# Performance work log

Measured on AMD Instinct MI355X. Metric: run time of the kernel, lower is better.

## Reference

```python
import jax, jax.numpy as jnp
import numpy as np
from jax import lax

EPS = 1e-6


def _gaussian_blur(heatmaps, kernel_size):
    # heatmaps: (B, K, H, W). 2D Gaussian conv with 'same' padding, as in the torch code.
    if kernel_size % 2 == 0:
        kernel_size += 1
    B, K, H, W = heatmaps.shape
    sigma = (kernel_size - 1) / 6.0
    coords = jnp.arange(kernel_size, dtype=heatmaps.dtype) - (kernel_size - 1) / 2.0
    g = jnp.exp(-coords ** 2 / (2 * sigma ** 2))
    g = g / g.sum()
    kernel = (g[None, :] * g[:, None])[None, None]  # (1,1,ks,ks)
    pad = kernel_size // 2
    x = heatmaps.reshape(B * K, 1, H, W)
    out = lax.conv_general_dilated(
        x, kernel, window_strides=(1, 1), padding=[(pad, pad), (pad, pad)],
        dimension_numbers=('NCHW', 'OIHW', 'NCHW'))
    return out.reshape(B, K, H, W)


def _dark_forward(heatmaps, kernel_size):
    B, K, H, W = heatmaps.shape
    smooth = _gaussian_blur(heatmaps, kernel_size)
    flat = smooth.reshape(B, K, H * W)
    max_idx = jnp.argmax(flat, axis=-1)            # (B,K) int
    max_vals = jnp.max(flat, axis=-1)              # (B,K)
    y_int = max_idx // W
    x_int = max_idx % W

    # Gather 3x3 patches around the peak (clipped indices; invalid peaks masked below).
    off = jnp.arange(-1, 2)
    yy = jnp.clip(y_int[..., None, None] + off[:, None], 0, H - 1)   # (B,K,3,3)
    xx = jnp.clip(x_int[..., None, None] + off[None, :], 0, W - 1)   # (B,K,3,3)
    lin = (yy * W + xx).reshape(B, K, 9)
    p = jnp.take_along_axis(flat, lin, axis=-1).reshape(B, K, 3, 3)

    dx = (p[..., 1, 2] - p[..., 1, 0]) * 0.5
    dy = (p[..., 2, 1] - p[..., 0, 1]) * 0.5
    dxx = p[..., 1, 2] - 2.0 * p[..., 1, 1] + p[..., 1, 0]
    dyy = p[..., 2, 1] - 2.0 * p[..., 1, 1] + p[..., 0, 1]
    dxy = (p[..., 2, 2] - p[..., 2, 0] - p[..., 0, 2] + p[..., 0, 0]) * 0.25
    det = dxx * dyy - dxy * dxy

    boundary_ok = (x_int >= 1) & (x_int < W - 1) & (y_int >= 1) & (y_int < H - 1)
    valid = boundary_ok & (jnp.abs(det) >= EPS) & (dxx < 0)
    safe_det = jnp.where(valid, det, 1.0)
    off_x = jnp.where(valid, jnp.clip(-(dyy * dx - dxy * dy) / safe_det, -0.5, 0.5), 0.0)
    off_y = jnp.where(valid, jnp.clip(-(dxx * dy - dxy * dx) / safe_det, -0.5, 0.5), 0.0)

    x = jnp.clip(x_int.astype(heatmaps.dtype) + off_x, 0, W - 1)
    y = jnp.clip(y_int.astype(heatmaps.dtype) + off_y, 0, H - 1)
    coords = jnp.stack([x, y], axis=-1)            # (B,K,2)
    return coords, max_vals


def setup_inputs() -> dict:
    key = jax.random.key(0)
    heatmaps = jax.random.normal(key, (64, 17, 256, 192), dtype=jnp.float32)
    return {"heatmaps": heatmaps, "kernel_size": 11}


def reference(heatmaps, kernel_size):
    return _dark_forward(heatmaps, kernel_size)
```

## Files before the change

kernel.cpp:

```cpp
#include <hip/hip_runtime.h>
#include <math.h>

#define H 256
#define W 192
#define BK 1088
#define KS 11
#define QROWS 64

struct GaussW { float g[KS]; };

__global__ __launch_bounds__(192) void dark_scan(const float* __restrict__ hm,
                                                 float* __restrict__ wsv,
                                                 int* __restrict__ wsi,
                                                 GaussW gw) {
  const int bid = blockIdx.x;
  const int q   = bid & 3;
  const int mg  = bid >> 2;
  const int t   = threadIdx.x;
  const int ml  = t / 48;
  const int cg  = t % 48;
  const int map = mg * 4 + ml;
  const int col0 = cg * 4;
  const float* base = hm + (size_t)map * (H * W);

  __shared__ float vbuf[4][208];
  __shared__ float rv[192];
  __shared__ int   ri[192];

  for (int i = t; i < 4 * 208; i += 192) ((float*)vbuf)[i] = 0.f;
  __syncthreads();

  const int y0 = q * QROWS;
  const int rs = (q == 0) ? 0 : (y0 - 5);
  const int re = y0 + QROWS + 4;

  float4 w[KS];
  #pragma unroll
  for (int i = 0; i < KS; ++i) w[i] = make_float4(0.f, 0.f, 0.f, 0.f);

  float bestv = -INFINITY;
  int   besti = 0x7fffffff;

  for (int rb = rs; rb <= re; rb += KS) {
    #pragma unroll
    for (int s = 0; s < KS; ++s) {
      const int rr = rb + s;
      if (rr <= re) {
        float4 raw;
        if (rr < H) raw = *(const float4*)(base + rr * W + col0);
        else        raw = make_float4(0.f, 0.f, 0.f, 0.f);
        w[s] = raw;
        if (rr >= y0 + 5) {
          float4 v = make_float4(0.f, 0.f, 0.f, 0.f);
          #pragma unroll
          for (int i = 0; i < KS; ++i) {
            const float4 wi = w[(s + 1 + i) % KS];
            const float gi = gw.g[i];
            v.x = fmaf(gi, wi.x, v.x);
            v.y = fmaf(gi, wi.y, v.y);
            v.z = fmaf(gi, wi.z, v.z);
            v.w = fmaf(gi, wi.w, v.w);
          }
          *(float4*)(&vbuf[ml][8 + col0]) = v;
          __syncthreads();
          const float* vb = &vbuf[ml][0];
          float a[20];
          *(float4*)(a + 0)  = *(const float4*)(vb + col0);
          *(float4*)(a + 4)  = *(const float4*)(vb + col0 + 4);
          *(float4*)(a + 8)  = *(const float4*)(vb + col0 + 8);
          *(float4*)(a + 12) = *(const float4*)(vb + col0 + 12);
          *(float4*)(a + 16) = *(const float4*)(vb + col0 + 16);
          const int y = rr - 5;
          #pragma unroll
          for (int c = 0; c < 4; ++c) {
            float hv = 0.f;
            #pragma unroll
            for (int j = 0; j < KS; ++j) hv = fmaf(gw.g[j], a[3 + c + j], hv);
            const int idx = y * W + col0 + c;
            if (hv > bestv) { bestv = hv; besti = idx; }
          }
          __syncthreads();
        }
      }
    }
  }

  rv[t] = bestv; ri[t] = besti;
  __syncthreads();
  if (cg == 0) {
    float bv = -INFINITY; int bi = 0x7fffffff;
    for (int k = 0; k < 48; ++k) {
      const float v = rv[ml * 48 + k]; const int ix = ri[ml * 48 + k];
      if (v > bv || (v == bv && ix < bi)) { bv = v; bi = ix; }
    }
    wsv[map * 4 + q] = bv;
    wsi[map * 4 + q] = bi;
  }
}

__global__ __launch_bounds__(64) void dark_decode(const float* __restrict__ hm,
                                                  const float* __restrict__ wsv,
                                                  const int* __restrict__ wsi,
                                                  float* __restrict__ out,
                                                  GaussW gw) {
  const int j = blockIdx.x;
  const int t = threadIdx.x;
  __shared__ float sv[4]; __shared__ int si[4];
  __shared__ float hbuf[39];
  __shared__ int sxy[3];
  __shared__ float sbv;

  if (t < 4) { sv[t] = wsv[j * 4 + t]; si[t] = wsi[j * 4 + t]; }
  __syncthreads();
  if (t == 0) {
    float bv = sv[0]; int bi = si[0];
    for (int k = 1; k < 4; ++k)
      if (sv[k] > bv || (sv[k] == bv && si[k] < bi)) { bv = sv[k]; bi = si[k]; }
    const int y = bi / W; const int x = bi - y * W;
    sxy[0] = x; sxy[1] = y;
    sxy[2] = (x >= 1 && x < W - 1 && y >= 1 && y < H - 1) ? 1 : 0;
    sbv = bv;
  }
  __syncthreads();
  const int x = sxy[0], y = sxy[1], interior = sxy[2];

  if (interior && t < 39) {
    const int rl = t / 3, dxc = t % 3;
    const int rr = y - 6 + rl;
    const int cc = x - 1 + dxc;
    float hv = 0.f;
    if (rr >= 0 && rr < H) {
      const float* rowp = hm + (size_t)j * (H * W) + rr * W;
      #pragma unroll
      for (int k = 0; k < KS; ++k) {
        const int c2 = cc - 5 + k;
        const float vv = (c2 >= 0 && c2 < W) ? rowp[c2] : 0.f;
        hv = fmaf(gw.g[k], vv, hv);
      }
    }
    hbuf[t] = hv;
  }
  __syncthreads();

  if (t == 0) {
    float xf = (float)x, yf = (float)y;
    if (interior) {
      float p[3][3];
      for (int dy = 0; dy < 3; ++dy)
        for (int dx = 0; dx < 3; ++dx) {
          float acc = 0.f;
          #pragma unroll
          for (int i = 0; i < KS; ++i) acc = fmaf(gw.g[i], hbuf[(dy + i) * 3 + dx], acc);
          p[dy][dx] = acc;
        }
      const float d1x = (p[1][2] - p[1][0]) * 0.5f;
      const float d1y = (p[2][1] - p[0][1]) * 0.5f;
      const float dxx = p[1][2] - 2.f * p[1][1] + p[1][0];
      const float dyy = p[2][1] - 2.f * p[1][1] + p[0][1];
      const float dxy = (p[2][2] - p[2][0] - p[0][2] + p[0][0]) * 0.25f;
      const float det = dxx * dyy - dxy * dxy;
      if (fabsf(det) >= 1e-6f && dxx < 0.f) {
        float ox = -(dyy * d1x - dxy * d1y) / det;
        float oy = -(dxx * d1y - dxy * d1x) / det;
        ox = fminf(fmaxf(ox, -0.5f), 0.5f);
        oy = fminf(fmaxf(oy, -0.5f), 0.5f);
        xf += ox; yf += oy;
      }
    }
    xf = fminf(fmaxf(xf, 0.f), (float)(W - 1));
    yf = fminf(fmaxf(yf, 0.f), (float)(H - 1));
    out[2 * j]     = xf;
    out[2 * j + 1] = yf;
    out[2 * BK + j] = sbv;
  }
}

extern "C" void kernel_launch(void* const* d_in, const int* in_sizes, int n_in,
                              void* d_out, int out_size, void* d_ws, size_t ws_size,
                              hipStream_t stream) {
  const float* hm = (const float*)d_in[0];
  float* out = (float*)d_out;
  float* wsv = (float*)d_ws;
  int*   wsi = (int*)d_ws + BK * 4;

  GaussW gw;
  {
    const double sig = (KS - 1) / 6.0;
    const float denom = (float)(2.0 * sig * sig);
    float g[KS]; float s = 0.f;
    for (int i = 0; i < KS; ++i) {
      const float c = (float)i - (float)((KS - 1) / 2);
      g[i] = expf(-(c * c) / denom);
      s += g[i];
    }
    for (int i = 0; i < KS; ++i) gw.g[i] = g[i] / s;
  }

  dark_scan<<<BK, 192, 0, stream>>>(hm, wsv, wsi, gw);
  dark_decode<<<BK, 64, 0, stream>>>(hm, wsv, wsi, out, gw);
}
```

Measured before the change: 321.7 us.

## Restructure blur scan to one wavefront per strip with shuffles instead of LDS barriers

Each 64-lane wavefront now owns one 32-row strip of a map, with 3 columns per lane. The horizontal blur pass gets its neighbour columns through cross-lane shuffles instead of a shared-memory row buffer with two block barriers per row. The next row is software-prefetched into registers, and the final argmax reduction uses xor shuffles. This removes per-row __syncthreads and LDS traffic, but the strips are shorter, so the overlapping halo reads grow, and the per-lane loads are scalar and unaligned rather than float4.

```diff
diff --git a/kernel.cpp b/kernel.cpp
--- a/kernel.cpp
+++ b/kernel.cpp
@@ -5,38 +5,35 @@
 #define W 192
 #define BK 1088
 #define KS 11
-#define QROWS 64
+#define NS 8
+#define SR 32
 
 struct GaussW { float g[KS]; };
 
-__global__ __launch_bounds__(192) void dark_scan(const float* __restrict__ hm,
+__device__ __forceinline__ float shflf(float v, int srcLane) {
+  return __shfl(v, srcLane & 63, 64);
+}
+
+__global__ __launch_bounds__(256) void dark_scan(const float* __restrict__ hm,
                                                  float* __restrict__ wsv,
                                                  int* __restrict__ wsi,
                                                  GaussW gw) {
-  const int bid = blockIdx.x;
-  const int q   = bid & 3;
-  const int mg  = bid >> 2;
-  const int t   = threadIdx.x;
-  const int ml  = t / 48;
-  const int cg  = t % 48;
-  const int map = mg * 4 + ml;
-  const int col0 = cg * 4;
-  const float* base = hm + (size_t)map * (H * W);
-
-  __shared__ float vbuf[4][208];
-  __shared__ float rv[192];
-  __shared__ int   ri[192];
-
-  for (int i = t; i < 4 * 208; i += 192) ((float*)vbuf)[i] = 0.f;
-  __syncthreads();
-
-  const int y0 = q * QROWS;
-  const int rs = (q == 0) ? 0 : (y0 - 5);
-  const int re = y0 + QROWS + 4;
-
-  float4 w[KS];
-  #pragma unroll
-  for (int i = 0; i < KS; ++i) w[i] = make_float4(0.f, 0.f, 0.f, 0.f);
+  const int wid  = (blockIdx.x << 2) + (threadIdx.x >> 6);
+  const int lane = threadIdx.x & 63;
+  const int map  = wid >> 3;
+  const int qs   = wid & 7;
+  const int y0   = qs * SR;
+  const int rs   = y0 - 5;
+  const int re   = y0 + SR + 4;
+  const float* base = hm + (size_t)map * (H * W) + 3 * lane;
+
+  float ring[KS][3];
+  float nxt0, nxt1, nxt2;
+
+  if (rs >= 0 && rs < H) {
+    const float* p = base + rs * W;
+    nxt0 = p[0]; nxt1 = p[1]; nxt2 = p[2];
+  } else { nxt0 = nxt1 = nxt2 = 0.f; }
 
   float bestv = -INFINITY;
   int   besti = 0x7fffffff;
@@ -46,55 +43,59 @@
     for (int s = 0; s < KS; ++s) {
       const int rr = rb + s;
       if (rr <= re) {
-        float4 raw;
-        if (rr < H) raw = *(const float4*)(base + rr * W + col0);
-        else        raw = make_float4(0.f, 0.f, 0.f, 0.f);
-        w[s] = raw;
+        ring[s][0] = nxt0; ring[s][1] = nxt1; ring[s][2] = nxt2;
+        {
+          const int nr = (rr < re) ? rr + 1 : -1;
+          if (nr >= 0 && nr < H) {
+            const float* p = base + nr * W;
+            nxt0 = p[0]; nxt1 = p[1]; nxt2 = p[2];
+          } else { nxt0 = nxt1 = nxt2 = 0.f; }
+        }
         if (rr >= y0 + 5) {
-          float4 v = make_float4(0.f, 0.f, 0.f, 0.f);
+          float v0 = 0.f, v1 = 0.f, v2 = 0.f;
           #pragma unroll
           for (int i = 0; i < KS; ++i) {
-            const float4 wi = w[(s + 1 + i) % KS];
+            const int sl2 = (s + 1 + i) % KS;
             const float gi = gw.g[i];
-            v.x = fmaf(gi, wi.x, v.x);
-            v.y = fmaf(gi, wi.y, v.y);
-            v.z = fmaf(gi, wi.z, v.z);
-            v.w = fmaf(gi, wi.w, v.w);
+            v0 = fmaf(gi, ring[sl2][0], v0);
+            v1 = fmaf(gi, ring[sl2][1], v1);
+            v2 = fmaf(gi, ring[sl2][2], v2);
           }
-          *(float4*)(&vbuf[ml][8 + col0]) = v;
-          __syncthreads();
-          const float* vb = &vbuf[ml][0];
-          float a[20];
-          *(float4*)(a + 0)  = *(const float4*)(vb + col0);
-          *(float4*)(a + 4)  = *(const float4*)(vb + col0 + 4);
-          *(float4*)(a + 8)  = *(const float4*)(vb + col0 + 8);
-          *(float4*)(a + 12) = *(const float4*)(vb + col0 + 12);
-          *(float4*)(a + 16) = *(const float4*)(vb + col0 + 16);
+          float w13[13];
+          w13[5] = v0; w13[6] = v1; w13[7] = v2;
+          const float m2b = shflf(v1, lane - 2), m2c = shflf(v2, lane - 2);
+          const float m1a = shflf(v0, lane - 1), m1b = shflf(v1, lane - 1), m1c = shflf(v2, lane - 1);
+          const float p1a = shflf(v0, lane + 1), p1b = shflf(v1, lane + 1), p1c = shflf(v2, lane + 1);
+          const float p2a = shflf(v0, lane + 2), p2b = shflf(v1, lane + 2);
+          const bool vm2 = (lane >= 2), vm1 = (lane >= 1);
+          const bool vp1 = (lane <= 62), vp2 = (lane <= 61);
+          w13[0]  = vm2 ? m2b : 0.f;  w13[1]  = vm2 ? m2c : 0.f;
+          w13[2]  = vm1 ? m1a : 0.f;  w13[3]  = vm1 ? m1b : 0.f;  w13[4] = vm1 ? m1c : 0.f;
+          w13[8]  = vp1 ? p1a : 0.f;  w13[9]  = vp1 ? p1b : 0.f;  w13[10] = vp1 ? p1c : 0.f;
+          w13[11] = vp2 ? p2a : 0.f;  w13[12] = vp2 ? p2b : 0.f;
           const int y = rr - 5;
           #pragma unroll
-          for (int c = 0; c < 4; ++c) {
+          for (int c = 0; c < 3; ++c) {
             float hv = 0.f;
             #pragma unroll
-            for (int j = 0; j < KS; ++j) hv = fmaf(gw.g[j], a[3 + c + j], hv);
-            const int idx = y * W + col0 + c;
+            for (int j = 0; j < KS; ++j) hv = fmaf(gw.g[j], w13[c + j], hv);
+            const int idx = y * W + 3 * lane + c;
             if (hv > bestv) { bestv = hv; besti = idx; }
           }
-          __syncthreads();
         }
       }
     }
   }
 
-  rv[t] = bestv; ri[t] = besti;
-  __syncthreads();
-  if (cg == 0) {
-    float bv = -INFINITY; int bi = 0x7fffffff;
-    for (int k = 0; k < 48; ++k) {
-      const float v = rv[ml * 48 + k]; const int ix = ri[ml * 48 + k];
-      if (v > bv || (v == bv && ix < bi)) { bv = v; bi = ix; }
-    }
-    wsv[map * 4 + q] = bv;
-    wsi[map * 4 + q] = bi;
+  #pragma unroll
+  for (int off = 32; off; off >>= 1) {
+    const float ov = __shfl_xor(bestv, off, 64);
+    const int   oi = __shfl_xor(besti, off, 64);
+    if (ov > bestv || (ov == bestv && oi < besti)) { bestv = ov; besti = oi; }
+  }
+  if (lane == 0) {
+    wsv[map * NS + qs] = bestv;
+    wsi[map * NS + qs] = besti;
   }
 }
 
@@ -105,16 +106,16 @@
                                                   GaussW gw) {
   const int j = blockIdx.x;
   const int t = threadIdx.x;
-  __shared__ float sv[4]; __shared__ int si[4];
+  __shared__ float sv[NS]; __shared__ int si[NS];
   __shared__ float hbuf[39];
   __shared__ int sxy[3];
   __shared__ float sbv;
 
-  if (t < 4) { sv[t] = wsv[j * 4 + t]; si[t] = wsi[j * 4 + t]; }
+  if (t < NS) { sv[t] = wsv[j * NS + t]; si[t] = wsi[j * NS + t]; }
   __syncthreads();
   if (t == 0) {
     float bv = sv[0]; int bi = si[0];
-    for (int k = 1; k < 4; ++k)
+    for (int k = 1; k < NS; ++k)
       if (sv[k] > bv || (sv[k] == bv && si[k] < bi)) { bv = sv[k]; bi = si[k]; }
     const int y = bi / W; const int x = bi - y * W;
     sxy[0] = x; sxy[1] = y;
@@ -181,7 +182,7 @@
   const float* hm = (const float*)d_in[0];
   float* out = (float*)d_out;
   float* wsv = (float*)d_ws;
-  int*   wsi = (int*)d_ws + BK * 4;
+  int*   wsi = (int*)d_ws + BK * NS;
 
   GaussW gw;
   {
@@ -196,6 +197,6 @@
     for (int i = 0; i < KS; ++i) gw.g[i] = g[i] / s;
   }
 
-  dark_scan<<<BK, 192, 0, stream>>>(hm, wsv, wsi, gw);
+  dark_scan<<<(BK * NS) / 4, 256, 0, stream>>>(hm, wsv, wsi, gw);
   dark_decode<<<BK, 64, 0, stream>>>(hm, wsv, wsi, out, gw);
 }
```

Result: no change. 325.0 us (+1.0%).
